# Optimization experiments

Hardware: AMD Instinct MI355X
Metric: run time of the kernel (lower is better)

The kernel has to match this reference:

```python
import jax, jax.numpy as jnp
import numpy as np

M = 28            # mask head resolution (mask_logit[i] is MxM)
NUM_CLASSES = 80  # max value of cls_idx (mask_image channel count)


def setup_inputs() -> dict:
    key = jax.random.key(0)
    k1, k2, k3, k4, k5, k6, k7 = jax.random.split(key, 7)
    N, H, W = 100, 800, 800
    cx = jax.random.uniform(k1, (N,), minval=0.0, maxval=float(W - 1))
    cy = jax.random.uniform(k2, (N,), minval=0.0, maxval=float(H - 1))
    bw = jax.random.uniform(k3, (N,), minval=20.0, maxval=300.0)
    bh = jax.random.uniform(k4, (N,), minval=20.0, maxval=300.0)
    mask_rois = jnp.stack([cx - bw / 2, cy - bh / 2, cx + bw / 2, cy + bh / 2], axis=1).astype(jnp.float32)
    cls_prob = jax.random.uniform(k5, (N,), dtype=jnp.float32)
    mask_prob = jax.random.normal(k6, (N, M, M), dtype=jnp.float32)
    cls_idx = jax.random.randint(k7, (N,), 1, NUM_CLASSES + 1, dtype=jnp.int32)
    return {"mask_rois": mask_rois, "cls_prob": cls_prob, "mask_prob": mask_prob,
            "cls_idx": cls_idx, "im_h": H, "im_w": W}


def _paste(logit, box, H, W):
    """Bilinear-paste an MxM logit into the full HxW image (== cv2.resize to (w,h)
    then placing at the box, evaluated directly on image pixel coords)."""
    x0, y0, x1, y1 = box[0], box[1], box[2], box[3]  # int32
    w = jnp.maximum(x1 - x0 + 1, 1).astype(jnp.float32)
    h = jnp.maximum(y1 - y0 + 1, 1).astype(jnp.float32)
    xs = jnp.arange(W, dtype=jnp.float32)
    ys = jnp.arange(H, dtype=jnp.float32)
    # cv2 bilinear mapping: src = (dst + 0.5) * (M / size) - 0.5, clamped at borders
    sx = jnp.clip((xs - x0.astype(jnp.float32) + 0.5) * (M / w) - 0.5, 0.0, M - 1.0)
    sy = jnp.clip((ys - y0.astype(jnp.float32) + 0.5) * (M / h) - 0.5, 0.0, M - 1.0)
    ix0 = jnp.floor(sx).astype(jnp.int32); ix1 = jnp.minimum(ix0 + 1, M - 1); fx = sx - ix0
    iy0 = jnp.floor(sy).astype(jnp.int32); iy1 = jnp.minimum(iy0 + 1, M - 1); fy = sy - iy0
    v00 = logit[iy0[:, None], ix0[None, :]]
    v01 = logit[iy0[:, None], ix1[None, :]]
    v10 = logit[iy1[:, None], ix0[None, :]]
    v11 = logit[iy1[:, None], ix1[None, :]]
    val = ((1 - fy)[:, None] * ((1 - fx)[None, :] * v00 + fx[None, :] * v01)
           + fy[:, None] * ((1 - fx)[None, :] * v10 + fx[None, :] * v11))
    xi = jnp.arange(W, dtype=jnp.int32)
    yi = jnp.arange(H, dtype=jnp.int32)
    inside_x = (xi >= jnp.maximum(x0, 0)) & (xi < jnp.minimum(x1 + 1, W))
    inside_y = (yi >= jnp.maximum(y0, 0)) & (yi < jnp.minimum(y1 + 1, H))
    inside = inside_y[:, None] & inside_x[None, :]
    return jnp.where(inside, val, 0.0), inside


def _forward(mask_rois, cls_prob, mask_prob, cls_idx, H, W, thr):
    N = mask_prob.shape[0]
    order = jnp.argsort(-cls_prob)                       # sort by score, descending
    boxes = mask_rois[order].astype(jnp.int32)
    logits = mask_prob[order]
    cls = cls_idx[order].astype(jnp.int32) - 1           # 0-based class ids
    pasted, inside = jax.vmap(lambda l, b: _paste(l, b, H, W))(logits, boxes)  # [N,H,W]

    def step(mask_image, xs):
        logit, ins, c = xs
        mask = (logit > 0) & ins                          # thresholded, in-image crop mask
        prev = mask_image[c]
        msum = jnp.sum(mask).astype(jnp.float32)
        ovl = jnp.sum(mask & prev).astype(jnp.float32)    # overlap with accumulated class mask
        keep = (msum > 0) & (ovl <= thr * msum)           # skip if ratio > threshold
        mask_image = mask_image.at[c].set(prev | (mask & keep))
        return mask_image, keep

    mask_image0 = jnp.zeros((NUM_CLASSES, H, W), dtype=bool)
    _, keep = jax.lax.scan(step, mask_image0, (pasted, inside, cls))

    # compact kept masks to the front (frame_id order); dropped boxes go to slot N (discarded)
    pos = jnp.where(keep, jnp.cumsum(keep.astype(jnp.int32)) - 1, N)
    energy = jnp.where(inside & keep[:, None, None], pasted, 0.0)
    full = jnp.zeros((N + 1, H, W), pasted.dtype).at[pos].set(energy)
    mask_energy = full[:N][None]                          # [1, N, H, W], kept masks first
    keep_inds = jnp.full((N + 1,), -1, jnp.int32).at[pos].set(
        jnp.where(keep, order.astype(jnp.int32), -1))[:N]
    return keep_inds, mask_energy


def reference(mask_rois, cls_prob, mask_prob, cls_idx, im_h, im_w):
    return _forward(mask_rois, cls_prob, mask_prob, cls_idx, int(im_h), int(im_w), 0.3)
```

## Files before the change

### kernel.cpp

```cpp
#include <hip/hip_runtime.h>

#define NINST 100
#define MLOG 28
#define IMG 800
#define LOGSZ (MLOG * MLOG)

#define OFF_ORDER 0
#define OFF_CLS   100
#define OFF_BOX   200
#define OFF_MSUM  600
#define OFF_SLOT  800
#define OFF_NK    900
#define OFF_NPAIR 901
#define OFF_MASK  1024
#define ROWW      12
#define MSTRIDE   (ROWW * 304)
#define OFF_PAIRS (OFF_MASK + NINST * MSTRIDE)
#define PAIR_CAP  512
#define ZTOT      (IMG * IMG * NINST / 4)
#define ZBLKS     4096

__global__ __launch_bounds__(256) void k_raster(const float* __restrict__ mask_prob,
                                                const float* __restrict__ cls_prob,
                                                const float* __restrict__ rois,
                                                const int* __restrict__ cls_idx,
                                                int* __restrict__ ws) {
    int b = blockIdx.x, tid = threadIdx.x;
    __shared__ float s_p[NINST];
    __shared__ int s_order[NINST];
    __shared__ float lg[LOGSZ];
    __shared__ int red[256];
    if (tid < NINST) s_p[tid] = cls_prob[tid];
    __syncthreads();
    if (tid < NINST) {
        float p = s_p[tid];
        int r = 0;
        for (int j = 0; j < NINST; j++) {
            float q = s_p[j];
            r += (q > p) || (q == p && j < tid);
        }
        s_order[r] = tid;
    }
    __syncthreads();
    int n = b;
    int orig = s_order[n];
    int x0 = (int)rois[4 * orig], y0 = (int)rois[4 * orig + 1];
    int x1 = (int)rois[4 * orig + 2], y1 = (int)rois[4 * orig + 3];
    if (b == 0) {
        if (tid == 0) ws[OFF_NPAIR] = 0;
        if (tid < NINST) {
            int o = s_order[tid];
            ws[OFF_ORDER + tid] = o;
            ws[OFF_CLS + tid] = cls_idx[o] - 1;
#pragma unroll
            for (int k = 0; k < 4; k++)
                ws[OFF_BOX + 4 * tid + k] = (int)rois[4 * o + k];
        }
    }
    for (int i = tid; i < LOGSZ; i += 256) lg[i] = mask_prob[orig * LOGSZ + i];
    __syncthreads();
    int xs = max(x0, 0), xe = min(x1 + 1, IMG);
    int ys = max(y0, 0), ye = min(y1 + 1, IMG);
    int wx0 = xs >> 5, nw = ((xe + 31) >> 5) - wx0, nrows = ye - ys;
    float wf = fmaxf((float)(x1 - x0 + 1), 1.f), hf = fmaxf((float)(y1 - y0 + 1), 1.f);
    float rx = 28.f / wf, ry = 28.f / hf;
    unsigned* mb = (unsigned*)(ws + OFF_MASK) + n * MSTRIDE;
    int total = nrows * nw, cnt = 0;
    for (int t = tid; t < total; t += 256) {
        int row = t / nw, wc = t - row * nw;
        int y = ys + row;
        float sy = ((float)y - (float)y0 + 0.5f) * ry - 0.5f;
        sy = fminf(fmaxf(sy, 0.f), 27.f);
        int iy0 = (int)sy, iy1 = min(iy0 + 1, 27);
        float fy = sy - (float)iy0;
        const float* r0 = lg + iy0 * MLOG;
        const float* r1 = lg + iy1 * MLOG;
        unsigned bits = 0u;
        int xbase = (wx0 + wc) << 5;
        int j0 = max(xs - xbase, 0), j1 = min(xe - xbase, 32);
        for (int j = j0; j < j1; j++) {
            int xx = xbase + j;
            float sx = ((float)xx - (float)x0 + 0.5f) * rx - 0.5f;
            sx = fminf(fmaxf(sx, 0.f), 27.f);
            int ix0 = (int)sx, ix1 = min(ix0 + 1, 27);
            float fx = sx - (float)ix0;
            float val = (1.f - fy) * ((1.f - fx) * r0[ix0] + fx * r0[ix1]) +
                        fy * ((1.f - fx) * r1[ix0] + fx * r1[ix1]);
            bits |= (val > 0.f) ? (1u << j) : 0u;
        }
        mb[row * ROWW + wc] = bits;
        cnt += __popc(bits);
    }
    red[tid] = cnt;
    __syncthreads();
    for (int s = 128; s; s >>= 1) {
        if (tid < s) red[tid] += red[tid + s];
        __syncthreads();
    }
    if (tid == 0) ws[OFF_MSUM + n] = red[0];
}

__global__ __launch_bounds__(64) void k_pairs(int* __restrict__ ws) {
    int i = blockIdx.x, j = blockIdx.y, tid = threadIdx.x;
    if (i >= j) return;
    if (ws[OFF_CLS + i] != ws[OFF_CLS + j]) return;
    if (ws[OFF_MSUM + i] == 0 || ws[OFF_MSUM + j] == 0) return;
    const int* bi = ws + OFF_BOX + 4 * i;
    const int* bj = ws + OFF_BOX + 4 * j;
    int ixs = max(bi[0], 0), ixe = min(bi[2] + 1, IMG);
    int iys = max(bi[1], 0), iye = min(bi[3] + 1, IMG);
    int jxs = max(bj[0], 0), jxe = min(bj[2] + 1, IMG);
    int jys = max(bj[1], 0), jye = min(bj[3] + 1, IMG);
    if (!(ixs < jxe && jxs < ixe && iys < jye && jys < iye)) return;
    int iwx0 = ixs >> 5, jwx0 = jxs >> 5;
    int wlo = max(iwx0, jwx0);
    int whi = min((ixe + 31) >> 5, (jxe + 31) >> 5);
    int rlo = max(iys, jys), rhi = min(iye, jye);
    int nw = whi - wlo, nrows = rhi - rlo;
    const unsigned* mi = (const unsigned*)(ws + OFF_MASK) + i * MSTRIDE;
    const unsigned* mj = (const unsigned*)(ws + OFF_MASK) + j * MSTRIDE;
    int total = nrows * nw, cnt = 0;
    for (int t = tid; t < total; t += 64) {
        int row = t / nw, wc = t - row * nw;
        int y = rlo + row, w = wlo + wc;
        unsigned a = mi[(y - iys) * ROWW + (w - iwx0)];
        unsigned b = mj[(y - jys) * ROWW + (w - jwx0)];
        cnt += __popc(a & b);
    }
    for (int off = 32; off; off >>= 1) cnt += __shfl_down(cnt, off);
    if (tid == 0) {
        int k = atomicAdd(ws + OFF_NPAIR, 1);
        if (k < PAIR_CAP) {
            ws[OFF_PAIRS + 3 * k] = i;
            ws[OFF_PAIRS + 3 * k + 1] = j;
            ws[OFF_PAIRS + 3 * k + 2] = cnt;
        }
    }
}

__global__ __launch_bounds__(256) void k_scan_zero(int* __restrict__ ws, float* __restrict__ out) {
    int b = blockIdx.x, tid = threadIdx.x;
    if (b > 0) {
        float4* z = (float4*)(out + NINST);
        for (size_t pi = (size_t)(b - 1) * 256 + tid; pi < (size_t)ZTOT; pi += (size_t)ZBLKS * 256)
            z[pi] = make_float4(0.f, 0.f, 0.f, 0.f);
        return;
    }
    if (tid >= 64) return;
    int lane = tid;
    const unsigned* maskbase = (const unsigned*)(ws + OFF_MASK);
    __shared__ int s_msum[NINST];
    __shared__ int s_box[4 * NINST];
    __shared__ int s_cand[32];
    for (int i = lane; i < NINST; i += 64) s_msum[i] = ws[OFF_MSUM + i];
    for (int i = lane; i < 4 * NINST; i += 64) s_box[i] = ws[OFF_BOX + i];
    int npair = min(ws[OFF_NPAIR], PAIR_CAP);
    int rpi[8], rpj[8], rpo[8];
#pragma unroll
    for (int s = 0; s < 8; s++) {
        int q = lane + (s << 6);
        rpi[s] = 0; rpo[s] = 0; rpj[s] = -1;
        if (q < npair) {
            rpi[s] = ws[OFF_PAIRS + 3 * q];
            rpj[s] = ws[OFF_PAIRS + 3 * q + 1];
            rpo[s] = ws[OFF_PAIRS + 3 * q + 2];
        }
    }
    asm volatile("s_waitcnt vmcnt(0) lgkmcnt(0)" ::: "memory");
    __builtin_amdgcn_sched_barrier(0);
    unsigned long long k0 = 0, k1 = 0;
    for (int n = 0; n < NINST; n++) {
        int msum = s_msum[n];
        int lsum = 0, lmax = 0, lcnt = 0;
#pragma unroll
        for (int s = 0; s < 8; s++) {
            if (rpj[s] == n) {
                int pi = rpi[s];
                bool kb = (pi < 64) ? ((k0 >> pi) & 1ull) : ((k1 >> (pi - 64)) & 1ull);
                if (kb) { lsum += rpo[s]; lmax = max(lmax, rpo[s]); lcnt++; }
            }
        }
        for (int off = 32; off; off >>= 1) {
            lsum += __shfl_xor(lsum, off);
            lmax = max(lmax, __shfl_xor(lmax, off));
            lcnt += __shfl_xor(lcnt, off);
        }
        float thr = 0.3f * (float)msum;
        int keep;
        if (lcnt == 0 || (float)lsum <= thr) keep = (msum > 0);
        else if ((float)lmax > thr) keep = 0;
        else {
            int nc = 0;
#pragma unroll
            for (int s = 0; s < 8; s++) {
                bool p = false; int piv = 0;
                if (rpj[s] == n) {
                    piv = rpi[s];
                    p = (piv < 64) ? ((k0 >> piv) & 1ull) : ((k1 >> (piv - 64)) & 1ull);
                }
                unsigned long long m = __ballot(p);
                int pos = nc + __popcll(m & ((1ull << lane) - 1ull));
                if (p && pos < 32) s_cand[pos] = piv;
                nc += __popcll(m);
            }
            nc = min(nc, 32);
            asm volatile("s_waitcnt lgkmcnt(0)" ::: "memory");
            __builtin_amdgcn_sched_barrier(0);
            int nxs = max(s_box[4 * n], 0), nxe = min(s_box[4 * n + 2] + 1, IMG);
            int nys = max(s_box[4 * n + 1], 0), nye = min(s_box[4 * n + 3] + 1, IMG);
            int wx0 = nxs >> 5, nwrd = ((nxe + 31) >> 5) - wx0, nrows = nye - nys;
            const unsigned* mn = maskbase + n * MSTRIDE;
            int total = nrows * nwrd, ovl = 0;
            for (int t2 = lane; t2 < total; t2 += 64) {
                int row = t2 / nwrd, wc = t2 - row * nwrd;
                unsigned bits = mn[row * ROWW + wc];
                if (!bits) continue;
                int y = nys + row, wa = wx0 + wc;
                unsigned img = 0;
                for (int k = 0; k < nc; k++) {
                    int m2 = s_cand[k];
                    int mys = max(s_box[4 * m2 + 1], 0), mye = min(s_box[4 * m2 + 3] + 1, IMG);
                    int mxs = max(s_box[4 * m2], 0), mxe = min(s_box[4 * m2 + 2] + 1, IMG);
                    int mwx0 = mxs >> 5, mnw = ((mxe + 31) >> 5) - mwx0;
                    int rr = y - mys, cc = wa - mwx0;
                    if (rr >= 0 && rr < (mye - mys) && cc >= 0 && cc < mnw)
                        img |= maskbase[m2 * MSTRIDE + rr * ROWW + cc];
                }
                ovl += __popc(bits & img);
            }
            for (int off = 32; off; off >>= 1) ovl += __shfl_xor(ovl, off);
            keep = (msum > 0) && ((float)ovl <= thr);
        }
        if (keep) { if (n < 64) k0 |= 1ull << n; else k1 |= 1ull << (n - 64); }
    }
    if (lane == 0) {
        int nk = 0;
        for (int n = 0; n < NINST; n++) {
            bool kb = (n < 64) ? ((k0 >> n) & 1ull) : ((k1 >> (n - 64)) & 1ull);
            if (kb) {
                ws[OFF_SLOT + nk] = n;
                out[nk] = (float)ws[OFF_ORDER + n];
                nk++;
            }
        }
        ws[OFF_NK] = nk;
        for (int s2 = nk; s2 < NINST; s2++) out[s2] = -1.f;
    }
}

__global__ __launch_bounds__(256) void k_box(const float* __restrict__ mask_prob,
                                             const int* __restrict__ ws,
                                             float* __restrict__ out) {
    int slot = blockIdx.y, tid = threadIdx.x;
    if (slot >= ws[OFF_NK]) return;
    int n = ws[OFF_SLOT + slot];
    const int* box = ws + OFF_BOX + 4 * n;
    int x0 = box[0], y0 = box[1], x1 = box[2], y1 = box[3];
    int xs = max(x0, 0), xe = min(x1 + 1, IMG);
    int ys = max(y0, 0), ye = min(y1 + 1, IMG);
    int xa = xs & ~3;
    int w4 = (xe - xa + 3) >> 2;
    int rows = ye - ys;
    int total = rows * w4;
    __shared__ float lg[LOGSZ];
    int orig = ws[OFF_ORDER + n];
    for (int i = tid; i < LOGSZ; i += 256) lg[i] = mask_prob[orig * LOGSZ + i];
    __syncthreads();
    float wf = fmaxf((float)(x1 - x0 + 1), 1.f), hf = fmaxf((float)(y1 - y0 + 1), 1.f);
    float rx = 28.f / wf, ry = 28.f / hf;
    float* base = out + NINST + (size_t)slot * (IMG * IMG);
    for (int t = blockIdx.x * 256 + tid; t < total; t += gridDim.x * 256) {
        int row = t / w4, c4 = t - row * w4;
        int y = ys + row, xb = xa + (c4 << 2);
        float sy = ((float)y - (float)y0 + 0.5f) * ry - 0.5f;
        sy = fminf(fmaxf(sy, 0.f), 27.f);
        int iy0 = (int)sy, iy1 = min(iy0 + 1, 27);
        float fy = sy - (float)iy0;
        const float* r0 = lg + iy0 * MLOG;
        const float* r1 = lg + iy1 * MLOG;
        float v[4];
#pragma unroll
        for (int j = 0; j < 4; j++) {
            int xx = xb + j;
            float val = 0.f;
            if (xx >= xs && xx < xe) {
                float sx = ((float)xx - (float)x0 + 0.5f) * rx - 0.5f;
                sx = fminf(fmaxf(sx, 0.f), 27.f);
                int ix0 = (int)sx, ix1 = min(ix0 + 1, 27);
                float fx = sx - (float)ix0;
                val = (1.f - fy) * ((1.f - fx) * r0[ix0] + fx * r0[ix1]) +
                      fy * ((1.f - fx) * r1[ix0] + fx * r1[ix1]);
            }
            v[j] = val;
        }
        *(float4*)(base + (size_t)y * IMG + xb) = make_float4(v[0], v[1], v[2], v[3]);
    }
}

extern "C" void kernel_launch(void* const* d_in, const int* in_sizes, int n_in,
                              void* d_out, int out_size, void* d_ws, size_t ws_size,
                              hipStream_t stream) {
    const float* rois      = (const float*)d_in[0];
    const float* cls_prob  = (const float*)d_in[1];
    const float* mask_prob = (const float*)d_in[2];
    const int*   cls_idx   = (const int*)d_in[3];
    int* ws = (int*)d_ws;
    float* out = (float*)d_out;

    k_raster<<<dim3(NINST), dim3(256), 0, stream>>>(mask_prob, cls_prob, rois, cls_idx, ws);
    k_pairs<<<dim3(NINST, NINST), dim3(64), 0, stream>>>(ws);
    k_scan_zero<<<dim3(1 + ZBLKS), dim3(256), 0, stream>>>(ws, out);
    k_box<<<dim3(91, NINST), dim3(256), 0, stream>>>(mask_prob, ws, out);
}
```

Baseline: 346.3 us.

## Enumerate candidate pairs in raster kernel and fuse overlap counting with zero-fill

Candidate same-class, box-overlapping pairs are now enumerated by block 0 of the raster kernel using shared-memory atomics. This removes the 100x100-block pair-checking launch. The bitmask overlap popcounts run on a fixed set of waves alongside the output zero-fill, and the greedy scan moves to its own single-block kernel. The risk is that the serial scan no longer overlaps the zero-fill, so it now sits on the critical path after the fill. Pairs whose mask sums are zero are no longer filtered at enumeration time.

```diff
diff --git a/kernel.cpp b/kernel.cpp
--- a/kernel.cpp
+++ b/kernel.cpp
@@ -18,7 +18,8 @@
 #define OFF_PAIRS (OFF_MASK + NINST * MSTRIDE)
 #define PAIR_CAP  512
 #define ZTOT      (IMG * IMG * NINST / 4)
-#define ZBLKS     4096
+#define PBLK      64
+#define ZBLKS     1984
 
 __global__ __launch_bounds__(256) void k_raster(const float* __restrict__ mask_prob,
                                                 const float* __restrict__ cls_prob,
@@ -30,6 +31,9 @@
     __shared__ int s_order[NINST];
     __shared__ float lg[LOGSZ];
     __shared__ int red[256];
+    __shared__ int s_c2[NINST];
+    __shared__ int s_b2[4 * NINST];
+    __shared__ int s_np;
     if (tid < NINST) s_p[tid] = cls_prob[tid];
     __syncthreads();
     if (tid < NINST) {
@@ -47,15 +51,38 @@
     int x0 = (int)rois[4 * orig], y0 = (int)rois[4 * orig + 1];
     int x1 = (int)rois[4 * orig + 2], y1 = (int)rois[4 * orig + 3];
     if (b == 0) {
-        if (tid == 0) ws[OFF_NPAIR] = 0;
+        if (tid == 0) s_np = 0;
         if (tid < NINST) {
             int o = s_order[tid];
+            int cv = cls_idx[o] - 1;
             ws[OFF_ORDER + tid] = o;
-            ws[OFF_CLS + tid] = cls_idx[o] - 1;
-#pragma unroll
-            for (int k = 0; k < 4; k++)
-                ws[OFF_BOX + 4 * tid + k] = (int)rois[4 * o + k];
-        }
+            ws[OFF_CLS + tid] = cv;
+            s_c2[tid] = cv;
+#pragma unroll
+            for (int k = 0; k < 4; k++) {
+                int bv = (int)rois[4 * o + k];
+                ws[OFF_BOX + 4 * tid + k] = bv;
+                s_b2[4 * tid + k] = bv;
+            }
+        }
+        __syncthreads();
+        for (int c = tid; c < NINST * NINST; c += 256) {
+            int i = c / NINST, j = c - i * NINST;
+            if (i >= j) continue;
+            if (s_c2[i] != s_c2[j]) continue;
+            int ixs = max(s_b2[4 * i], 0), ixe = min(s_b2[4 * i + 2] + 1, IMG);
+            int iys = max(s_b2[4 * i + 1], 0), iye = min(s_b2[4 * i + 3] + 1, IMG);
+            int jxs = max(s_b2[4 * j], 0), jxe = min(s_b2[4 * j + 2] + 1, IMG);
+            int jys = max(s_b2[4 * j + 1], 0), jye = min(s_b2[4 * j + 3] + 1, IMG);
+            if (!(ixs < jxe && jxs < ixe && iys < jye && jys < iye)) continue;
+            int k = atomicAdd(&s_np, 1);
+            if (k < PAIR_CAP) {
+                ws[OFF_PAIRS + 3 * k] = i;
+                ws[OFF_PAIRS + 3 * k + 1] = j;
+            }
+        }
+        __syncthreads();
+        if (tid == 0) ws[OFF_NPAIR] = min(s_np, PAIR_CAP);
     }
     for (int i = tid; i < LOGSZ; i += 256) lg[i] = mask_prob[orig * LOGSZ + i];
     __syncthreads();
@@ -100,54 +127,47 @@
     if (tid == 0) ws[OFF_MSUM + n] = red[0];
 }
 
-__global__ __launch_bounds__(64) void k_pairs(int* __restrict__ ws) {
-    int i = blockIdx.x, j = blockIdx.y, tid = threadIdx.x;
-    if (i >= j) return;
-    if (ws[OFF_CLS + i] != ws[OFF_CLS + j]) return;
-    if (ws[OFF_MSUM + i] == 0 || ws[OFF_MSUM + j] == 0) return;
-    const int* bi = ws + OFF_BOX + 4 * i;
-    const int* bj = ws + OFF_BOX + 4 * j;
-    int ixs = max(bi[0], 0), ixe = min(bi[2] + 1, IMG);
-    int iys = max(bi[1], 0), iye = min(bi[3] + 1, IMG);
-    int jxs = max(bj[0], 0), jxe = min(bj[2] + 1, IMG);
-    int jys = max(bj[1], 0), jye = min(bj[3] + 1, IMG);
-    if (!(ixs < jxe && jxs < ixe && iys < jye && jys < iye)) return;
-    int iwx0 = ixs >> 5, jwx0 = jxs >> 5;
-    int wlo = max(iwx0, jwx0);
-    int whi = min((ixe + 31) >> 5, (jxe + 31) >> 5);
-    int rlo = max(iys, jys), rhi = min(iye, jye);
-    int nw = whi - wlo, nrows = rhi - rlo;
-    const unsigned* mi = (const unsigned*)(ws + OFF_MASK) + i * MSTRIDE;
-    const unsigned* mj = (const unsigned*)(ws + OFF_MASK) + j * MSTRIDE;
-    int total = nrows * nw, cnt = 0;
-    for (int t = tid; t < total; t += 64) {
-        int row = t / nw, wc = t - row * nw;
-        int y = rlo + row, w = wlo + wc;
-        unsigned a = mi[(y - iys) * ROWW + (w - iwx0)];
-        unsigned b = mj[(y - jys) * ROWW + (w - jwx0)];
-        cnt += __popc(a & b);
-    }
-    for (int off = 32; off; off >>= 1) cnt += __shfl_down(cnt, off);
-    if (tid == 0) {
-        int k = atomicAdd(ws + OFF_NPAIR, 1);
-        if (k < PAIR_CAP) {
-            ws[OFF_PAIRS + 3 * k] = i;
-            ws[OFF_PAIRS + 3 * k + 1] = j;
-            ws[OFF_PAIRS + 3 * k + 2] = cnt;
-        }
-    }
-}
-
-__global__ __launch_bounds__(256) void k_scan_zero(int* __restrict__ ws, float* __restrict__ out) {
+__global__ __launch_bounds__(256) void k_pairs_zero(int* __restrict__ ws, float* __restrict__ out) {
     int b = blockIdx.x, tid = threadIdx.x;
-    if (b > 0) {
+    if (b >= PBLK) {
         float4* z = (float4*)(out + NINST);
-        for (size_t pi = (size_t)(b - 1) * 256 + tid; pi < (size_t)ZTOT; pi += (size_t)ZBLKS * 256)
+        for (size_t pi = (size_t)(b - PBLK) * 256 + tid; pi < (size_t)ZTOT; pi += (size_t)ZBLKS * 256)
             z[pi] = make_float4(0.f, 0.f, 0.f, 0.f);
         return;
     }
-    if (tid >= 64) return;
-    int lane = tid;
+    int npair = min(ws[OFF_NPAIR], PAIR_CAP);
+    int wid = (b << 2) | (tid >> 6), lane = tid & 63;
+    const unsigned* maskbase = (const unsigned*)(ws + OFF_MASK);
+    for (int k = wid; k < npair; k += (PBLK << 2)) {
+        int i = ws[OFF_PAIRS + 3 * k], j = ws[OFF_PAIRS + 3 * k + 1];
+        const int* bi = ws + OFF_BOX + 4 * i;
+        const int* bj = ws + OFF_BOX + 4 * j;
+        int ixs = max(bi[0], 0), ixe = min(bi[2] + 1, IMG);
+        int iys = max(bi[1], 0), iye = min(bi[3] + 1, IMG);
+        int jxs = max(bj[0], 0), jxe = min(bj[2] + 1, IMG);
+        int jys = max(bj[1], 0), jye = min(bj[3] + 1, IMG);
+        int iwx0 = ixs >> 5, jwx0 = jxs >> 5;
+        int wlo = max(iwx0, jwx0);
+        int whi = min((ixe + 31) >> 5, (jxe + 31) >> 5);
+        int rlo = max(iys, jys), rhi = min(iye, jye);
+        int nw = whi - wlo, nrows = rhi - rlo;
+        const unsigned* mi = maskbase + i * MSTRIDE;
+        const unsigned* mj = maskbase + j * MSTRIDE;
+        int total = nrows * nw, cnt = 0;
+        for (int t = lane; t < total; t += 64) {
+            int row = t / nw, wc = t - row * nw;
+            int y = rlo + row, w = wlo + wc;
+            unsigned a = mi[(y - iys) * ROWW + (w - iwx0)];
+            unsigned bb = mj[(y - jys) * ROWW + (w - jwx0)];
+            cnt += __popc(a & bb);
+        }
+        for (int off = 32; off; off >>= 1) cnt += __shfl_down(cnt, off);
+        if (lane == 0) ws[OFF_PAIRS + 3 * k + 2] = cnt;
+    }
+}
+
+__global__ __launch_bounds__(64) void k_scan(int* __restrict__ ws, float* __restrict__ out) {
+    int lane = threadIdx.x;
     const unsigned* maskbase = (const unsigned*)(ws + OFF_MASK);
     __shared__ int s_msum[NINST];
     __shared__ int s_box[4 * NINST];
@@ -308,7 +328,7 @@
     float* out = (float*)d_out;
 
     k_raster<<<dim3(NINST), dim3(256), 0, stream>>>(mask_prob, cls_prob, rois, cls_idx, ws);
-    k_pairs<<<dim3(NINST, NINST), dim3(64), 0, stream>>>(ws);
-    k_scan_zero<<<dim3(1 + ZBLKS), dim3(256), 0, stream>>>(ws, out);
+    k_pairs_zero<<<dim3(PBLK + ZBLKS), dim3(256), 0, stream>>>(ws, out);
+    k_scan<<<dim3(1), dim3(64), 0, stream>>>(ws, out);
     k_box<<<dim3(91, NINST), dim3(256), 0, stream>>>(mask_prob, ws, out);
 }
```

After: 384.1 us. 10.9% more time.
